# Kernel optimization log

Hardware: AMD Instinct MI355X
Metric: run time of the kernel (lower is better)

The kernel has to match this reference:

```python
import jax, jax.numpy as jnp
import numpy as np

WH, WW = 8, 8
N_TOK = WH * WW
NUM_HEADS = 4
DIM = 128
B_WIN = 4096  # num_windows * B
NW = 64       # windows per image (for mask)


def _make_rel_tables():
    # relative coords table (1, 2*Wh-1, 2*Ww-1, 2), log-spaced as in SwinV2
    ch = np.arange(-(WH - 1), WH, dtype=np.float32)
    cw = np.arange(-(WW - 1), WW, dtype=np.float32)
    t = np.stack(np.meshgrid(ch, cw, indexing='ij'), axis=-1)[None]  # (1,15,15,2)
    t[..., 0] /= (WH - 1)
    t[..., 1] /= (WW - 1)
    t *= 8
    t = np.sign(t) * np.log2(np.abs(t) + 1.0) / np.log2(8)
    # relative position index (N, N)
    coords = np.stack(np.meshgrid(np.arange(WH), np.arange(WW), indexing='ij'))
    cf = coords.reshape(2, -1)
    rel = cf[:, :, None] - cf[:, None, :]
    rel = rel.transpose(1, 2, 0).copy()
    rel[:, :, 0] += WH - 1
    rel[:, :, 1] += WW - 1
    rel[:, :, 0] *= 2 * WW - 1
    idx = rel.sum(-1).astype(np.int32)
    return jnp.asarray(t), jnp.asarray(idx)


def setup_inputs() -> dict:
    key = jax.random.key(0)
    ks = jax.random.split(key, 8)
    table, idx = _make_rel_tables()
    return {
        'x': jax.random.normal(ks[0], (B_WIN, N_TOK, DIM), jnp.float32),
        'context': jax.random.normal(ks[1], (B_WIN, N_TOK, DIM), jnp.float32),
        'mask': jnp.zeros((NW, N_TOK, N_TOK), jnp.float32),
        'q_w': jax.random.normal(ks[2], (DIM, DIM), jnp.float32) * 0.02,
        'q_b': jnp.zeros((DIM,), jnp.float32),
        'kv_w': jax.random.normal(ks[3], (2 * DIM, DIM), jnp.float32) * 0.02,
        'v_b': jnp.zeros((DIM,), jnp.float32),
        'logit_scale': jnp.full((NUM_HEADS, 1, 1), np.log(10.0), jnp.float32),
        'cpb_w1': jax.random.normal(ks[4], (512, 2), jnp.float32) * 0.02,
        'cpb_b1': jnp.zeros((512,), jnp.float32),
        'cpb_w2': jax.random.normal(ks[5], (NUM_HEADS, 512), jnp.float32) * 0.02,
        'proj_w': jax.random.normal(ks[6], (DIM, DIM), jnp.float32) * 0.02,
        'proj_b': jnp.zeros((DIM,), jnp.float32),
        'rel_coords_table': table,
        'rel_pos_index': idx,
    }


def _l2norm(t, eps=1e-12):
    return t / jnp.maximum(jnp.linalg.norm(t, axis=-1, keepdims=True), eps)


def reference(x, context, mask, q_w, q_b, kv_w, v_b, logit_scale,
              cpb_w1, cpb_b1, cpb_w2, proj_w, proj_b,
              rel_coords_table, rel_pos_index):
    B_, N, C = x.shape
    H = NUM_HEADS
    hd = C // H
    # projections (kv bias = [zeros_like(v_b); v_b])
    q = x @ q_w.T + q_b
    kv_bias = jnp.concatenate([jnp.zeros_like(v_b), v_b])
    kv = context @ kv_w.T + kv_bias
    q = q.reshape(B_, N, H, hd).transpose(0, 2, 1, 3)          # (B_,H,N,hd)
    kv = kv.reshape(B_, N, 2, H, hd).transpose(2, 0, 3, 1, 4)  # (2,B_,H,N,hd)
    k, v = kv[0], kv[1]
    # cosine attention with clamped learned scale
    attn = jnp.einsum('bhnd,bhmd->bhnm', _l2norm(q), _l2norm(k))
    scale = jnp.exp(jnp.minimum(logit_scale, np.log(1.0 / 0.01)))  # (H,1,1)
    attn = attn * scale[None]
    # CPB-MLP relative position bias
    hidd = jax.nn.relu(rel_coords_table @ cpb_w1.T + cpb_b1)   # (1,15,15,512)
    table = (hidd @ cpb_w2.T).reshape(-1, H)                   # ((2Wh-1)(2Ww-1), H)
    bias = table[rel_pos_index.reshape(-1)].reshape(N, N, H)
    bias = 16.0 * jax.nn.sigmoid(bias.transpose(2, 0, 1))      # (H,N,N)
    attn = attn + bias[None]
    # shift mask
    nW = mask.shape[0]
    attn = attn.reshape(B_ // nW, nW, H, N, N) + mask[None, :, None]
    attn = attn.reshape(B_, H, N, N)
    attn = jax.nn.softmax(attn, axis=-1)
    out = jnp.einsum('bhnm,bhmd->bhnd', attn, v)
    out = out.transpose(0, 2, 1, 3).reshape(B_, N, C)
    return out @ proj_w.T + proj_b
```

## Files before the change

kernel.cpp:

```cpp
#include <hip/hip_runtime.h>
#include <hip/hip_bf16.h>

#define NT 64
#define DIM 128

typedef __attribute__((ext_vector_type(8))) short short8;
typedef __attribute__((ext_vector_type(4))) short short4v;
typedef __attribute__((ext_vector_type(8))) __bf16 bf16x8;
typedef __attribute__((ext_vector_type(4))) float floatx4;

#define MFMA(a,b,c) __builtin_amdgcn_mfma_f32_16x16x32_bf16(a,b,c,0,0,0)
#define SWZ(idx, row) ((idx) ^ (((row)&7)<<3))

__device__ __forceinline__ short bfbits(float f) {
  return __builtin_bit_cast(short, (__bf16)f);
}

__device__ __forceinline__ bf16x8 frag_bf(const short* __restrict__ p) {
  return __builtin_bit_cast(bf16x8, *(const short8*)p);
}

__device__ __forceinline__ short8 pack8(float4 a, float4 b) {
  short8 v;
  v[0]=bfbits(a.x); v[1]=bfbits(a.y); v[2]=bfbits(a.z); v[3]=bfbits(a.w);
  v[4]=bfbits(b.x); v[5]=bfbits(b.y); v[6]=bfbits(b.z); v[7]=bfbits(b.w);
  return v;
}

__global__ void prep_kernel(const float* __restrict__ table,
                            const float* __restrict__ w1,
                            const float* __restrict__ b1,
                            const float* __restrict__ w2,
                            const int*   __restrict__ idx,
                            const float* __restrict__ q_w,
                            const float* __restrict__ kv_w,
                            const float* __restrict__ proj_w,
                            float* __restrict__ bias_packed,
                            short* __restrict__ wbf) {
  int t = threadIdx.x;
  if (blockIdx.x == 0) {
    __shared__ float logits[225][4];
    if (t < 225) {
      float t0 = table[2*t], t1 = table[2*t+1];
      float a0=0.f, a1=0.f, a2=0.f, a3=0.f;
      for (int j = 0; j < 512; ++j) {
        float h = fmaxf(0.f, t0 * w1[2*j] + t1 * w1[2*j+1] + b1[j]);
        a0 += h * w2[j];
        a1 += h * w2[512 + j];
        a2 += h * w2[1024 + j];
        a3 += h * w2[1536 + j];
      }
      logits[t][0]=a0; logits[t][1]=a1; logits[t][2]=a2; logits[t][3]=a3;
    }
    __syncthreads();
    for (int f = t; f < 16384; f += 256) {
      int i    = f & 3;
      int lane = (f >> 2) & 63;
      int nt   = (f >> 8) & 3;
      int mt   = (f >> 10) & 3;
      int h    = (f >> 12) & 3;
      int r = mt*16 + (lane >> 4)*4 + i;
      int c = nt*16 + (lane & 15);
      int p = idx[r*64 + c];
      float v = logits[p][h];
      bias_packed[f] = 16.f / (1.f + __expf(-v));
    }
  } else {
    int gidx = (blockIdx.x - 1) * 4096 + t * 16;
    const float* src; int off;
    if (gidx < 16384)      { src = q_w;    off = gidx; }
    else if (gidx < 49152) { src = kv_w;   off = gidx - 16384; }
    else                   { src = proj_w; off = gidx - 49152; }
    const float4* s = (const float4*)(src + off);
    short* dst = wbf + gidx;
#pragma unroll
    for (int i = 0; i < 2; ++i)
      *(short8*)(dst + i*8) = pack8(s[2*i], s[2*i+1]);
  }
}

__global__ __launch_bounds__(512, 4)
void swin_ctx_attn_kernel(const float* __restrict__ x, const float* __restrict__ ctx,
                          const float* __restrict__ mask,
                          const short* __restrict__ wq, const float* __restrict__ q_b,
                          const short* __restrict__ wkv, const float* __restrict__ v_b,
                          const float* __restrict__ logit_scale,
                          const short* __restrict__ wproj, const float* __restrict__ proj_b,
                          const float* __restrict__ bias_p,
                          float* __restrict__ out) {
  __shared__ short lds[40960] __attribute__((aligned(16)));
  const int tid  = threadIdx.x;
  const int lane = tid & 63;
  const int wv   = tid >> 6;
  const int h    = wv >> 1;
  const int s    = wv & 1;
  const int b    = blockIdx.x;
  const int lr   = lane & 15;
  const int lg   = lane >> 4;

  short* sx     = lds;
  short* scx    = lds + 8192;
  short* qn     = lds + 16384 + h*6144;
  short* kn     = qn + 2048;
  short* vT     = qn + 4096;
  short* attnb  = qn;
  short* outp_l = sx;

  const float* xw = x   + (size_t)b*(NT*DIM);
  const float* cw = ctx + (size_t)b*(NT*DIM);

  {
    const int sr = tid >> 3, sc0 = (tid & 7) * 16;
    const float4* xs = (const float4*)(xw + sr*DIM + sc0);
    const float4* cs = (const float4*)(cw + sr*DIM + sc0);
    float4 xr[4], cr[4];
#pragma unroll
    for (int i = 0; i < 4; ++i) xr[i] = xs[i];
#pragma unroll
    for (int i = 0; i < 4; ++i) cr[i] = cs[i];
#pragma unroll
    for (int i = 0; i < 2; ++i)
      *(short8*)(sx + SWZ(sr*128 + sc0 + i*8, sr)) = pack8(xr[2*i], xr[2*i+1]);
#pragma unroll
    for (int i = 0; i < 2; ++i)
      *(short8*)(scx + SWZ(sr*128 + sc0 + i*8, sr)) = pack8(cr[2*i], cr[2*i+1]);
  }
  bf16x8 Bq[4][2];
#pragma unroll
  for (int ks = 0; ks < 4; ++ks)
#pragma unroll
    for (int n = 0; n < 2; ++n)
      Bq[ks][n] = frag_bf(wq + (h*32 + n*16 + lr)*DIM + ks*32 + lg*8);
  __syncthreads();

  {
    floatx4 acc[2][2] = {};
    for (int ks = 0; ks < 4; ++ks) {
      bf16x8 A[2];
#pragma unroll
      for (int m = 0; m < 2; ++m) {
        int q = s*32 + m*16 + lr;
        A[m] = frag_bf(sx + SWZ(q*128 + ks*32 + lg*8, q));
      }
#pragma unroll
      for (int n = 0; n < 2; ++n)
#pragma unroll
        for (int m = 0; m < 2; ++m)
          acc[m][n] = MFMA(A[m], Bq[ks][n], acc[m][n]);
    }
    float qb0 = q_b[h*32 + lr], qb1 = q_b[h*32 + 16 + lr];
#pragma unroll
    for (int m = 0; m < 2; ++m) {
      floatx4 ss;
#pragma unroll
      for (int i = 0; i < 4; ++i) {
        acc[m][0][i] += qb0; acc[m][1][i] += qb1;
        ss[i] = acc[m][0][i]*acc[m][0][i] + acc[m][1][i]*acc[m][1][i];
      }
      for (int mm = 1; mm < 16; mm <<= 1)
#pragma unroll
        for (int i = 0; i < 4; ++i) ss[i] += __shfl_xor(ss[i], mm, 64);
#pragma unroll
      for (int i = 0; i < 4; ++i) {
        float sc = 1.0f / fmaxf(sqrtf(ss[i]), 1e-12f);
        int row = s*32 + m*16 + lg*4 + i;
        qn[SWZ(row*32 + lr,      row)] = bfbits(acc[m][0][i] * sc);
        qn[SWZ(row*32 + 16 + lr, row)] = bfbits(acc[m][1][i] * sc);
      }
    }
  }

  {
    floatx4 kacc[2][2] = {}, vacc[2][2] = {};
    for (int ks = 0; ks < 4; ++ks) {
      bf16x8 A[2], Bk[2], Bv[2];
#pragma unroll
      for (int m = 0; m < 2; ++m) {
        int q = s*32 + m*16 + lr;
        A[m] = frag_bf(scx + SWZ(q*128 + ks*32 + lg*8, q));
      }
#pragma unroll
      for (int n = 0; n < 2; ++n) {
        Bk[n] = frag_bf(wkv + (h*32 + n*16 + lr)*DIM + ks*32 + lg*8);
        Bv[n] = frag_bf(wkv + (DIM + h*32 + n*16 + lr)*DIM + ks*32 + lg*8);
      }
#pragma unroll
      for (int n = 0; n < 2; ++n)
#pragma unroll
        for (int m = 0; m < 2; ++m) {
          kacc[m][n] = MFMA(A[m], Bk[n], kacc[m][n]);
          vacc[m][n] = MFMA(A[m], Bv[n], vacc[m][n]);
        }
    }
#pragma unroll
    for (int m = 0; m < 2; ++m) {
      floatx4 ss;
#pragma unroll
      for (int i = 0; i < 4; ++i)
        ss[i] = kacc[m][0][i]*kacc[m][0][i] + kacc[m][1][i]*kacc[m][1][i];
      for (int mm = 1; mm < 16; mm <<= 1)
#pragma unroll
        for (int i = 0; i < 4; ++i) ss[i] += __shfl_xor(ss[i], mm, 64);
#pragma unroll
      for (int i = 0; i < 4; ++i) {
        float sc = 1.0f / fmaxf(sqrtf(ss[i]), 1e-12f);
        int row = s*32 + m*16 + lg*4 + i;
        kn[SWZ(row*32 + lr,      row)] = bfbits(kacc[m][0][i] * sc);
        kn[SWZ(row*32 + 16 + lr, row)] = bfbits(kacc[m][1][i] * sc);
      }
    }
    float vb0 = v_b[h*32 + lr], vb1 = v_b[h*32 + 16 + lr];
#pragma unroll
    for (int m = 0; m < 2; ++m)
#pragma unroll
      for (int n = 0; n < 2; ++n) {
        float vb = n ? vb1 : vb0;
        short4v s4;
#pragma unroll
        for (int i = 0; i < 4; ++i) s4[i] = bfbits(vacc[m][n][i] + vb);
        int d = n*16 + lr, tok0 = s*32 + m*16 + lg*4;
        *(short4v*)(vT + SWZ(d*64 + tok0, d)) = s4;
      }
  }
  __syncthreads();

  floatx4 sacc[2][4] = {};
  {
    bf16x8 A[2], Bf[4];
#pragma unroll
    for (int m = 0; m < 2; ++m) {
      int q = s*32 + m*16 + lr;
      A[m] = frag_bf(qn + SWZ(q*32 + lg*8, q));
    }
#pragma unroll
    for (int n = 0; n < 4; ++n) {
      int r = n*16 + lr;
      Bf[n] = frag_bf(kn + SWZ(r*32 + lg*8, r));
    }
#pragma unroll
    for (int n = 0; n < 4; ++n)
#pragma unroll
      for (int m = 0; m < 2; ++m)
        sacc[m][n] = MFMA(A[m], Bf[n], sacc[m][n]);
  }

  {
    float scl = __expf(fminf(logit_scale[h], 4.605170185988091f));
    int wimg = b & 63;
#pragma unroll
    for (int m = 0; m < 2; ++m)
#pragma unroll
      for (int nt = 0; nt < 4; ++nt) {
        floatx4 bias4 = ((const floatx4*)bias_p)[(h*16 + (s*2+m)*4 + nt)*64 + lane];
#pragma unroll
        for (int i = 0; i < 4; ++i) {
          int r = s*32 + m*16 + lg*4 + i, c = nt*16 + lr;
          sacc[m][nt][i] = sacc[m][nt][i]*scl + bias4[i] + mask[((size_t)wimg*64 + r)*64 + c];
        }
      }
#pragma unroll
    for (int m = 0; m < 2; ++m) {
      floatx4 rmax;
#pragma unroll
      for (int i = 0; i < 4; ++i)
        rmax[i] = fmaxf(fmaxf(sacc[m][0][i], sacc[m][1][i]), fmaxf(sacc[m][2][i], sacc[m][3][i]));
      for (int mm = 1; mm < 16; mm <<= 1)
#pragma unroll
        for (int i = 0; i < 4; ++i) rmax[i] = fmaxf(rmax[i], __shfl_xor(rmax[i], mm, 64));
      floatx4 rsum = {};
#pragma unroll
      for (int nt = 0; nt < 4; ++nt)
#pragma unroll
        for (int i = 0; i < 4; ++i) {
          sacc[m][nt][i] = __expf(sacc[m][nt][i] - rmax[i]);
          rsum[i] += sacc[m][nt][i];
        }
      for (int mm = 1; mm < 16; mm <<= 1)
#pragma unroll
        for (int i = 0; i < 4; ++i) rsum[i] += __shfl_xor(rsum[i], mm, 64);
#pragma unroll
      for (int i = 0; i < 4; ++i) rsum[i] = 1.0f / rsum[i];
#pragma unroll
      for (int nt = 0; nt < 4; ++nt)
#pragma unroll
        for (int i = 0; i < 4; ++i) sacc[m][nt][i] *= rsum[i];
    }
  }
  __syncthreads();

#pragma unroll
  for (int m = 0; m < 2; ++m)
#pragma unroll
    for (int nt = 0; nt < 4; ++nt)
#pragma unroll
      for (int i = 0; i < 4; ++i) {
        int q = s*32 + m*16 + lg*4 + i;
        attnb[SWZ(q*64 + nt*16 + lr, q)] = bfbits(sacc[m][nt][i]);
      }
  asm volatile("s_waitcnt lgkmcnt(0)" ::: "memory");
  __builtin_amdgcn_sched_barrier(0);

  floatx4 oacc[2][2] = {};
#pragma unroll
  for (int ks = 0; ks < 2; ++ks) {
    bf16x8 A[2], Bf[2];
#pragma unroll
    for (int m = 0; m < 2; ++m) {
      int q = s*32 + m*16 + lr;
      A[m] = frag_bf(attnb + SWZ(q*64 + ks*32 + lg*8, q));
    }
#pragma unroll
    for (int n = 0; n < 2; ++n) {
      int d = n*16 + lr;
      Bf[n] = frag_bf(vT + SWZ(d*64 + ks*32 + lg*8, d));
    }
#pragma unroll
    for (int n = 0; n < 2; ++n)
#pragma unroll
      for (int m = 0; m < 2; ++m)
        oacc[m][n] = MFMA(A[m], Bf[n], oacc[m][n]);
  }

#pragma unroll
  for (int m = 0; m < 2; ++m)
#pragma unroll
    for (int n = 0; n < 2; ++n)
#pragma unroll
      for (int i = 0; i < 4; ++i) {
        int q = s*32 + m*16 + lg*4 + i;
        outp_l[SWZ(q*128 + h*32 + n*16 + lr, q)] = bfbits(oacc[m][n][i]);
      }
  __syncthreads();

  {
    floatx4 acc[2][2] = {};
    for (int ks = 0; ks < 4; ++ks) {
      bf16x8 A[2], B[2];
#pragma unroll
      for (int m = 0; m < 2; ++m) {
        int q = s*32 + m*16 + lr;
        A[m] = frag_bf(outp_l + SWZ(q*128 + ks*32 + lg*8, q));
      }
#pragma unroll
      for (int n = 0; n < 2; ++n)
        B[n] = frag_bf(wproj + (h*32 + n*16 + lr)*DIM + ks*32 + lg*8);
#pragma unroll
      for (int n = 0; n < 2; ++n)
#pragma unroll
        for (int m = 0; m < 2; ++m)
          acc[m][n] = MFMA(A[m], B[n], acc[m][n]);
    }
    float pb0 = proj_b[h*32 + lr], pb1 = proj_b[h*32 + 16 + lr];
    float* outp = out + (size_t)b * (NT*DIM);
#pragma unroll
    for (int m = 0; m < 2; ++m)
#pragma unroll
      for (int n = 0; n < 2; ++n) {
        float pb = n ? pb1 : pb0;
#pragma unroll
        for (int i = 0; i < 4; ++i)
          outp[(s*32 + m*16 + lg*4 + i)*DIM + h*32 + n*16 + lr] = acc[m][n][i] + pb;
      }
  }
}

extern "C" void kernel_launch(void* const* d_in, const int* in_sizes, int n_in,
                              void* d_out, int out_size, void* d_ws, size_t ws_size,
                              hipStream_t stream) {
  const float* x     = (const float*)d_in[0];
  const float* ctx   = (const float*)d_in[1];
  const float* mask  = (const float*)d_in[2];
  const float* q_w   = (const float*)d_in[3];
  const float* q_b   = (const float*)d_in[4];
  const float* kv_w  = (const float*)d_in[5];
  const float* v_b   = (const float*)d_in[6];
  const float* ls    = (const float*)d_in[7];
  const float* w1    = (const float*)d_in[8];
  const float* b1    = (const float*)d_in[9];
  const float* w2    = (const float*)d_in[10];
  const float* pw    = (const float*)d_in[11];
  const float* pb    = (const float*)d_in[12];
  const float* table = (const float*)d_in[13];
  const int*   idx   = (const int*)d_in[14];

  float* bias_p = (float*)d_ws;
  short* wbf    = (short*)((char*)d_ws + 65536);
  short* wq     = wbf;
  short* wkv    = wbf + 16384;
  short* wproj  = wbf + 49152;
  int B = in_sizes[0] / (NT * DIM);

  prep_kernel<<<17, 256, 0, stream>>>(table, w1, b1, w2, idx, q_w, kv_w, pw,
                                      bias_p, wbf);
  swin_ctx_attn_kernel<<<B, 512, 0, stream>>>(x, ctx, mask, wq, q_b, wkv, v_b,
                                              ls, wproj, pb, bias_p, (float*)d_out);
}
```

Before: 267.3 us.

## Compute attention transposed with register-resident Q and P to shrink LDS

The kernel now computes Q and scores in transposed form (W·X^T, K·Q^T), so normalized Q and the softmax probabilities stay in registers and are repacked into MFMA operands with cross-lane shuffles and byte permutes instead of round-tripping through LDS. The logit scale is folded into the Q normalization, the row-sum reciprocal is applied after the PV product, and bias/mask loads become vectorized to match the new layout. LDS shrinks from 80KB to 48KB by reusing the x/context buffers for V^T and the attention output, and launch bounds rise to 6 blocks per SM. The cost is extra shuffles and register pressure under the tighter occupancy target, plus an additional barrier.

```diff
diff --git a/kernel.cpp b/kernel.cpp
--- a/kernel.cpp
+++ b/kernel.cpp
@@ -8,6 +8,7 @@
 typedef __attribute__((ext_vector_type(4))) short short4v;
 typedef __attribute__((ext_vector_type(8))) __bf16 bf16x8;
 typedef __attribute__((ext_vector_type(4))) float floatx4;
+typedef __attribute__((ext_vector_type(4))) unsigned uintx4;
 
 #define MFMA(a,b,c) __builtin_amdgcn_mfma_f32_16x16x32_bf16(a,b,c,0,0,0)
 #define SWZ(idx, row) ((idx) ^ (((row)&7)<<3))
@@ -15,11 +16,13 @@
 __device__ __forceinline__ short bfbits(float f) {
   return __builtin_bit_cast(short, (__bf16)f);
 }
-
+__device__ __forceinline__ unsigned pk2(float lo, float hi) {
+  return (unsigned)(unsigned short)__builtin_bit_cast(unsigned short, (__bf16)lo)
+       | ((unsigned)(unsigned short)__builtin_bit_cast(unsigned short, (__bf16)hi) << 16);
+}
 __device__ __forceinline__ bf16x8 frag_bf(const short* __restrict__ p) {
   return __builtin_bit_cast(bf16x8, *(const short8*)p);
 }
-
 __device__ __forceinline__ short8 pack8(float4 a, float4 b) {
   short8 v;
   v[0]=bfbits(a.x); v[1]=bfbits(a.y); v[2]=bfbits(a.z); v[3]=bfbits(a.w);
@@ -56,12 +59,12 @@
     for (int f = t; f < 16384; f += 256) {
       int i    = f & 3;
       int lane = (f >> 2) & 63;
-      int nt   = (f >> 8) & 3;
-      int mt   = (f >> 10) & 3;
-      int h    = (f >> 12) & 3;
-      int r = mt*16 + (lane >> 4)*4 + i;
-      int c = nt*16 + (lane & 15);
-      int p = idx[r*64 + c];
+      int qt   = (f >> 8) & 3;
+      int mk   = (f >> 10) & 3;
+      int h    = f >> 12;
+      int q = qt*16 + (lane & 15);
+      int k = mk*16 + ((lane >> 4) & 3)*4 + i;
+      int p = idx[q*64 + k];
       float v = logits[p][h];
       bias_packed[f] = 16.f / (1.f + __expf(-v));
     }
@@ -79,7 +82,7 @@
   }
 }
 
-__global__ __launch_bounds__(512, 4)
+__global__ __launch_bounds__(512, 6)
 void swin_ctx_attn_kernel(const float* __restrict__ x, const float* __restrict__ ctx,
                           const float* __restrict__ mask,
                           const short* __restrict__ wq, const float* __restrict__ q_b,
@@ -88,7 +91,7 @@
                           const short* __restrict__ wproj, const float* __restrict__ proj_b,
                           const float* __restrict__ bias_p,
                           float* __restrict__ out) {
-  __shared__ short lds[40960] __attribute__((aligned(16)));
+  __shared__ short lds[24576] __attribute__((aligned(16)));
   const int tid  = threadIdx.x;
   const int lane = tid & 63;
   const int wv   = tid >> 6;
@@ -98,13 +101,12 @@
   const int lr   = lane & 15;
   const int lg   = lane >> 4;
 
-  short* sx     = lds;
-  short* scx    = lds + 8192;
-  short* qn     = lds + 16384 + h*6144;
-  short* kn     = qn + 2048;
-  short* vT     = qn + 4096;
-  short* attnb  = qn;
-  short* outp_l = sx;
+  short* xb   = lds;
+  short* cb   = lds + 8192;
+  short* kn   = lds + 16384;
+  short* vT   = xb;
+  short* outp = cb;
+  short* knh  = kn + h*2048;
 
   const float* xw = x   + (size_t)b*(NT*DIM);
   const float* cw = ctx + (size_t)b*(NT*DIM);
@@ -120,238 +122,244 @@
     for (int i = 0; i < 4; ++i) cr[i] = cs[i];
 #pragma unroll
     for (int i = 0; i < 2; ++i)
-      *(short8*)(sx + SWZ(sr*128 + sc0 + i*8, sr)) = pack8(xr[2*i], xr[2*i+1]);
+      *(short8*)(xb + SWZ(sr*128 + sc0 + i*8, sr)) = pack8(xr[2*i], xr[2*i+1]);
 #pragma unroll
     for (int i = 0; i < 2; ++i)
-      *(short8*)(scx + SWZ(sr*128 + sc0 + i*8, sr)) = pack8(cr[2*i], cr[2*i+1]);
-  }
-  bf16x8 Bq[4][2];
-#pragma unroll
-  for (int ks = 0; ks < 4; ++ks)
-#pragma unroll
-    for (int n = 0; n < 2; ++n)
-      Bq[ks][n] = frag_bf(wq + (h*32 + n*16 + lr)*DIM + ks*32 + lg*8);
+      *(short8*)(cb + SWZ(sr*128 + sc0 + i*8, sr)) = pack8(cr[2*i], cr[2*i+1]);
+  }
   __syncthreads();
 
-  {
-    floatx4 acc[2][2] = {};
+  const int sA = ((lane & 16) << 1) | (lane & 15);
+  const int sB = sA + 16;
+  const unsigned selp = (lane & 32) ? 0x07060302u : 0x05040100u;
+
+  bf16x8 qB[2];
+  float scl = __expf(fminf(logit_scale[h], 4.605170185988091f));
+  {
+    floatx4 aq[2][2] = {};
     for (int ks = 0; ks < 4; ++ks) {
-      bf16x8 A[2];
+      bf16x8 xf[2], wf[2];
+#pragma unroll
+      for (int n = 0; n < 2; ++n) {
+        int tok = (2*s + n)*16 + lr;
+        xf[n] = frag_bf(xb + SWZ(tok*128 + ks*32 + lg*8, tok));
+      }
+#pragma unroll
+      for (int mc = 0; mc < 2; ++mc)
+        wf[mc] = frag_bf(wq + (h*32 + mc*16 + lr)*DIM + ks*32 + lg*8);
+#pragma unroll
+      for (int mc = 0; mc < 2; ++mc)
+#pragma unroll
+        for (int n = 0; n < 2; ++n)
+          aq[mc][n] = MFMA(wf[mc], xf[n], aq[mc][n]);
+    }
+    floatx4 qb4[2];
+#pragma unroll
+    for (int mc = 0; mc < 2; ++mc)
+      qb4[mc] = *(const floatx4*)(q_b + h*32 + mc*16 + lg*4);
+#pragma unroll
+    for (int n = 0; n < 2; ++n) {
+      float ss = 0.f;
+#pragma unroll
+      for (int mc = 0; mc < 2; ++mc)
+#pragma unroll
+        for (int i = 0; i < 4; ++i) {
+          aq[mc][n][i] += qb4[mc][i];
+          ss += aq[mc][n][i]*aq[mc][n][i];
+        }
+      ss += __shfl_xor(ss, 16, 64);
+      ss += __shfl_xor(ss, 32, 64);
+      float sc = scl / fmaxf(sqrtf(ss), 1e-12f);
+#pragma unroll
+      for (int mc = 0; mc < 2; ++mc)
+#pragma unroll
+        for (int i = 0; i < 4; ++i) aq[mc][n][i] *= sc;
+      unsigned pq[4], w[8];
+#pragma unroll
+      for (int i = 0; i < 4; ++i) pq[i] = pk2(aq[0][n][i], aq[1][n][i]);
+#pragma unroll
+      for (int j = 0; j < 8; ++j) w[j] = __shfl(pq[j & 3], (j < 4) ? sA : sB, 64);
+      uintx4 u;
+#pragma unroll
+      for (int t = 0; t < 4; ++t) u[t] = __builtin_amdgcn_perm(w[2*t+1], w[2*t], selp);
+      qB[n] = __builtin_bit_cast(bf16x8, u);
+    }
+  }
+
+  floatx4 ak[2][2] = {}, av[2][2] = {};
+  for (int ks = 0; ks < 4; ++ks) {
+    bf16x8 cf[2], wkf[2], wvf[2];
+#pragma unroll
+    for (int r = 0; r < 2; ++r) {
+      int tok = (2*s + r)*16 + lr;
+      cf[r] = frag_bf(cb + SWZ(tok*128 + ks*32 + lg*8, tok));
+    }
+#pragma unroll
+    for (int mc = 0; mc < 2; ++mc) {
+      wkf[mc] = frag_bf(wkv + (h*32 + mc*16 + lr)*DIM + ks*32 + lg*8);
+      wvf[mc] = frag_bf(wkv + (DIM + h*32 + mc*16 + lr)*DIM + ks*32 + lg*8);
+    }
+#pragma unroll
+    for (int mc = 0; mc < 2; ++mc)
+#pragma unroll
+      for (int n = 0; n < 2; ++n) {
+        ak[mc][n] = MFMA(wkf[mc], cf[n], ak[mc][n]);
+        av[mc][n] = MFMA(cf[mc], wvf[n], av[mc][n]);
+      }
+  }
+#pragma unroll
+  for (int n = 0; n < 2; ++n) {
+    float ss = 0.f;
+#pragma unroll
+    for (int mc = 0; mc < 2; ++mc)
+#pragma unroll
+      for (int i = 0; i < 4; ++i) ss += ak[mc][n][i]*ak[mc][n][i];
+    ss += __shfl_xor(ss, 16, 64);
+    ss += __shfl_xor(ss, 32, 64);
+    float sc = 1.0f / fmaxf(sqrtf(ss), 1e-12f);
+#pragma unroll
+    for (int mc = 0; mc < 2; ++mc)
+#pragma unroll
+      for (int i = 0; i < 4; ++i) ak[mc][n][i] *= sc;
+  }
+#pragma unroll
+  for (int mc = 0; mc < 2; ++mc)
+#pragma unroll
+    for (int n = 0; n < 2; ++n) {
+      int tok = (2*s + n)*16 + lr;
+      short4v t4;
+#pragma unroll
+      for (int i = 0; i < 4; ++i) t4[i] = bfbits(ak[mc][n][i]);
+      *(short4v*)(knh + SWZ(tok*32 + mc*16 + lg*4, tok)) = t4;
+    }
+  __syncthreads();
+
+  {
+    float vb0 = v_b[h*32 + lr], vb1 = v_b[h*32 + 16 + lr];
+#pragma unroll
+    for (int m = 0; m < 2; ++m)
+#pragma unroll
+      for (int n = 0; n < 2; ++n) {
+        int chG = h*32 + n*16 + lr;
+        float vb = n ? vb1 : vb0;
+        short4v t4;
+#pragma unroll
+        for (int i = 0; i < 4; ++i) t4[i] = bfbits(av[m][n][i] + vb);
+        *(short4v*)(vT + SWZ(chG*64 + s*32 + m*16 + lg*4, chG)) = t4;
+      }
+  }
+  __syncthreads();
+
+  floatx4 st[4][2] = {};
+  {
+    bf16x8 kf[4];
+#pragma unroll
+    for (int mk = 0; mk < 4; ++mk) {
+      int tok = mk*16 + lr;
+      kf[mk] = frag_bf(knh + SWZ(tok*32 + lg*8, tok));
+    }
+#pragma unroll
+    for (int mk = 0; mk < 4; ++mk)
+#pragma unroll
+      for (int n = 0; n < 2; ++n)
+        st[mk][n] = MFMA(kf[mk], qB[n], st[mk][n]);
+  }
+
+  float rinv[2];
+  {
+    int wimg = b & 63;
+#pragma unroll
+    for (int n = 0; n < 2; ++n) {
+      int qcol = (2*s + n)*16 + lr;
+#pragma unroll
+      for (int mk = 0; mk < 4; ++mk) {
+        floatx4 b4 = ((const floatx4*)bias_p)[((h*4 + mk)*4 + (2*s + n))*64 + lane];
+        floatx4 m4 = *(const floatx4*)(mask + ((size_t)wimg*64 + qcol)*64 + mk*16 + lg*4);
+#pragma unroll
+        for (int i = 0; i < 4; ++i) st[mk][n][i] += b4[i] + m4[i];
+      }
+      float mx = st[0][n][0];
+#pragma unroll
+      for (int mk = 0; mk < 4; ++mk)
+#pragma unroll
+        for (int i = 0; i < 4; ++i) mx = fmaxf(mx, st[mk][n][i]);
+      mx = fmaxf(mx, __shfl_xor(mx, 16, 64));
+      mx = fmaxf(mx, __shfl_xor(mx, 32, 64));
+      float sum = 0.f;
+#pragma unroll
+      for (int mk = 0; mk < 4; ++mk)
+#pragma unroll
+        for (int i = 0; i < 4; ++i) {
+          st[mk][n][i] = __expf(st[mk][n][i] - mx);
+          sum += st[mk][n][i];
+        }
+      sum += __shfl_xor(sum, 16, 64);
+      sum += __shfl_xor(sum, 32, 64);
+      rinv[n] = 1.0f / sum;
+    }
+  }
+
+  floatx4 ot[2][2] = {};
+#pragma unroll
+  for (int kk = 0; kk < 2; ++kk) {
+    bf16x8 pB[2];
+#pragma unroll
+    for (int n = 0; n < 2; ++n) {
+      unsigned pp[4], w[8];
+#pragma unroll
+      for (int i = 0; i < 4; ++i) pp[i] = pk2(st[2*kk][n][i], st[2*kk+1][n][i]);
+#pragma unroll
+      for (int j = 0; j < 8; ++j) w[j] = __shfl(pp[j & 3], (j < 4) ? sA : sB, 64);
+      uintx4 u;
+#pragma unroll
+      for (int t = 0; t < 4; ++t) u[t] = __builtin_amdgcn_perm(w[2*t+1], w[2*t], selp);
+      pB[n] = __builtin_bit_cast(bf16x8, u);
+    }
+    bf16x8 vf[2];
+#pragma unroll
+    for (int mo = 0; mo < 2; ++mo) {
+      int chG = h*32 + mo*16 + lr;
+      vf[mo] = frag_bf(vT + SWZ(chG*64 + kk*32 + lg*8, chG));
+    }
+#pragma unroll
+    for (int mo = 0; mo < 2; ++mo)
+#pragma unroll
+      for (int n = 0; n < 2; ++n)
+        ot[mo][n] = MFMA(vf[mo], pB[n], ot[mo][n]);
+  }
+
+#pragma unroll
+  for (int mo = 0; mo < 2; ++mo)
+#pragma unroll
+    for (int n = 0; n < 2; ++n) {
+      int tok = (2*s + n)*16 + lr;
+      short4v t4;
+#pragma unroll
+      for (int i = 0; i < 4; ++i) t4[i] = bfbits(ot[mo][n][i] * rinv[n]);
+      *(short4v*)(outp + SWZ(tok*128 + h*32 + mo*16 + lg*4, tok)) = t4;
+    }
+  __syncthreads();
+
+  {
+    floatx4 ap[2][2] = {};
+    for (int ks = 0; ks < 4; ++ks) {
+      bf16x8 of[2], wpf[2];
 #pragma unroll
       for (int m = 0; m < 2; ++m) {
-        int q = s*32 + m*16 + lr;
-        A[m] = frag_bf(sx + SWZ(q*128 + ks*32 + lg*8, q));
+        int tok = s*32 + m*16 + lr;
+        of[m] = frag_bf(outp + SWZ(tok*128 + ks*32 + lg*8, tok));
       }
 #pragma unroll
       for (int n = 0; n < 2; ++n)
-#pragma unroll
-        for (int m = 0; m < 2; ++m)
-          acc[m][n] = MFMA(A[m], Bq[ks][n], acc[m][n]);
-    }
-    float qb0 = q_b[h*32 + lr], qb1 = q_b[h*32 + 16 + lr];
-#pragma unroll
-    for (int m = 0; m < 2; ++m) {
-      floatx4 ss;
-#pragma unroll
-      for (int i = 0; i < 4; ++i) {
-        acc[m][0][i] += qb0; acc[m][1][i] += qb1;
-        ss[i] = acc[m][0][i]*acc[m][0][i] + acc[m][1][i]*acc[m][1][i];
-      }
-      for (int mm = 1; mm < 16; mm <<= 1)
-#pragma unroll
-        for (int i = 0; i < 4; ++i) ss[i] += __shfl_xor(ss[i], mm, 64);
-#pragma unroll
-      for (int i = 0; i < 4; ++i) {
-        float sc = 1.0f / fmaxf(sqrtf(ss[i]), 1e-12f);
-        int row = s*32 + m*16 + lg*4 + i;
-        qn[SWZ(row*32 + lr,      row)] = bfbits(acc[m][0][i] * sc);
-        qn[SWZ(row*32 + 16 + lr, row)] = bfbits(acc[m][1][i] * sc);
-      }
-    }
-  }
-
-  {
-    floatx4 kacc[2][2] = {}, vacc[2][2] = {};
-    for (int ks = 0; ks < 4; ++ks) {
-      bf16x8 A[2], Bk[2], Bv[2];
-#pragma unroll
-      for (int m = 0; m < 2; ++m) {
-        int q = s*32 + m*16 + lr;
-        A[m] = frag_bf(scx + SWZ(q*128 + ks*32 + lg*8, q));
-      }
-#pragma unroll
-      for (int n = 0; n < 2; ++n) {
-        Bk[n] = frag_bf(wkv + (h*32 + n*16 + lr)*DIM + ks*32 + lg*8);
-        Bv[n] = frag_bf(wkv + (DIM + h*32 + n*16 + lr)*DIM + ks*32 + lg*8);
-      }
-#pragma unroll
-      for (int n = 0; n < 2; ++n)
-#pragma unroll
-        for (int m = 0; m < 2; ++m) {
-          kacc[m][n] = MFMA(A[m], Bk[n], kacc[m][n]);
-          vacc[m][n] = MFMA(A[m], Bv[n], vacc[m][n]);
-        }
-    }
-#pragma unroll
-    for (int m = 0; m < 2; ++m) {
-      floatx4 ss;
-#pragma unroll
-      for (int i = 0; i < 4; ++i)
-        ss[i] = kacc[m][0][i]*kacc[m][0][i] + kacc[m][1][i]*kacc[m][1][i];
-      for (int mm = 1; mm < 16; mm <<= 1)
-#pragma unroll
-        for (int i = 0; i < 4; ++i) ss[i] += __shfl_xor(ss[i], mm, 64);
-#pragma unroll
-      for (int i = 0; i < 4; ++i) {
-        float sc = 1.0f / fmaxf(sqrtf(ss[i]), 1e-12f);
-        int row = s*32 + m*16 + lg*4 + i;
-        kn[SWZ(row*32 + lr,      row)] = bfbits(kacc[m][0][i] * sc);
-        kn[SWZ(row*32 + 16 + lr, row)] = bfbits(kacc[m][1][i] * sc);
-      }
-    }
-    float vb0 = v_b[h*32 + lr], vb1 = v_b[h*32 + 16 + lr];
-#pragma unroll
-    for (int m = 0; m < 2; ++m)
-#pragma unroll
-      for (int n = 0; n < 2; ++n) {
-        float vb = n ? vb1 : vb0;
-        short4v s4;
-#pragma unroll
-        for (int i = 0; i < 4; ++i) s4[i] = bfbits(vacc[m][n][i] + vb);
-        int d = n*16 + lr, tok0 = s*32 + m*16 + lg*4;
-        *(short4v*)(vT + SWZ(d*64 + tok0, d)) = s4;
-      }
-  }
-  __syncthreads();
-
-  floatx4 sacc[2][4] = {};
-  {
-    bf16x8 A[2], Bf[4];
-#pragma unroll
-    for (int m = 0; m < 2; ++m) {
-      int q = s*32 + m*16 + lr;
-      A[m] = frag_bf(qn + SWZ(q*32 + lg*8, q));
-    }
-#pragma unroll
-    for (int n = 0; n < 4; ++n) {
-      int r = n*16 + lr;
-      Bf[n] = frag_bf(kn + SWZ(r*32 + lg*8, r));
-    }
-#pragma unroll
-    for (int n = 0; n < 4; ++n)
+        wpf[n] = frag_bf(wproj + (h*32 + n*16 + lr)*DIM + ks*32 + lg*8);
 #pragma unroll
       for (int m = 0; m < 2; ++m)
-        sacc[m][n] = MFMA(A[m], Bf[n], sacc[m][n]);
-  }
-
-  {
-    float scl = __expf(fminf(logit_scale[h], 4.605170185988091f));
-    int wimg = b & 63;
-#pragma unroll
-    for (int m = 0; m < 2; ++m)
-#pragma unroll
-      for (int nt = 0; nt < 4; ++nt) {
-        floatx4 bias4 = ((const floatx4*)bias_p)[(h*16 + (s*2+m)*4 + nt)*64 + lane];
-#pragma unroll
-        for (int i = 0; i < 4; ++i) {
-          int r = s*32 + m*16 + lg*4 + i, c = nt*16 + lr;
-          sacc[m][nt][i] = sacc[m][nt][i]*scl + bias4[i] + mask[((size_t)wimg*64 + r)*64 + c];
-        }
-      }
-#pragma unroll
-    for (int m = 0; m < 2; ++m) {
-      floatx4 rmax;
-#pragma unroll
-      for (int i = 0; i < 4; ++i)
-        rmax[i] = fmaxf(fmaxf(sacc[m][0][i], sacc[m][1][i]), fmaxf(sacc[m][2][i], sacc[m][3][i]));
-      for (int mm = 1; mm < 16; mm <<= 1)
-#pragma unroll
-        for (int i = 0; i < 4; ++i) rmax[i] = fmaxf(rmax[i], __shfl_xor(rmax[i], mm, 64));
-      floatx4 rsum = {};
-#pragma unroll
-      for (int nt = 0; nt < 4; ++nt)
-#pragma unroll
-        for (int i = 0; i < 4; ++i) {
-          sacc[m][nt][i] = __expf(sacc[m][nt][i] - rmax[i]);
-          rsum[i] += sacc[m][nt][i];
-        }
-      for (int mm = 1; mm < 16; mm <<= 1)
-#pragma unroll
-        for (int i = 0; i < 4; ++i) rsum[i] += __shfl_xor(rsum[i], mm, 64);
-#pragma unroll
-      for (int i = 0; i < 4; ++i) rsum[i] = 1.0f / rsum[i];
-#pragma unroll
-      for (int nt = 0; nt < 4; ++nt)
-#pragma unroll
-        for (int i = 0; i < 4; ++i) sacc[m][nt][i] *= rsum[i];
-    }
-  }
-  __syncthreads();
-
-#pragma unroll
-  for (int m = 0; m < 2; ++m)
-#pragma unroll
-    for (int nt = 0; nt < 4; ++nt)
-#pragma unroll
-      for (int i = 0; i < 4; ++i) {
-        int q = s*32 + m*16 + lg*4 + i;
-        attnb[SWZ(q*64 + nt*16 + lr, q)] = bfbits(sacc[m][nt][i]);
-      }
-  asm volatile("s_waitcnt lgkmcnt(0)" ::: "memory");
-  __builtin_amdgcn_sched_barrier(0);
-
-  floatx4 oacc[2][2] = {};
-#pragma unroll
-  for (int ks = 0; ks < 2; ++ks) {
-    bf16x8 A[2], Bf[2];
-#pragma unroll
-    for (int m = 0; m < 2; ++m) {
-      int q = s*32 + m*16 + lr;
-      A[m] = frag_bf(attnb + SWZ(q*64 + ks*32 + lg*8, q));
-    }
-#pragma unroll
-    for (int n = 0; n < 2; ++n) {
-      int d = n*16 + lr;
-      Bf[n] = frag_bf(vT + SWZ(d*64 + ks*32 + lg*8, d));
-    }
-#pragma unroll
-    for (int n = 0; n < 2; ++n)
-#pragma unroll
-      for (int m = 0; m < 2; ++m)
-        oacc[m][n] = MFMA(A[m], Bf[n], oacc[m][n]);
-  }
-
-#pragma unroll
-  for (int m = 0; m < 2; ++m)
-#pragma unroll
-    for (int n = 0; n < 2; ++n)
-#pragma unroll
-      for (int i = 0; i < 4; ++i) {
-        int q = s*32 + m*16 + lg*4 + i;
-        outp_l[SWZ(q*128 + h*32 + n*16 + lr, q)] = bfbits(oacc[m][n][i]);
-      }
-  __syncthreads();
-
-  {
-    floatx4 acc[2][2] = {};
-    for (int ks = 0; ks < 4; ++ks) {
-      bf16x8 A[2], B[2];
-#pragma unroll
-      for (int m = 0; m < 2; ++m) {
-        int q = s*32 + m*16 + lr;
-        A[m] = frag_bf(outp_l + SWZ(q*128 + ks*32 + lg*8, q));
-      }
-#pragma unroll
-      for (int n = 0; n < 2; ++n)
-        B[n] = frag_bf(wproj + (h*32 + n*16 + lr)*DIM + ks*32 + lg*8);
-#pragma unroll
-      for (int n = 0; n < 2; ++n)
-#pragma unroll
-        for (int m = 0; m < 2; ++m)
-          acc[m][n] = MFMA(A[m], B[n], acc[m][n]);
+#pragma unroll
+        for (int n = 0; n < 2; ++n)
+          ap[m][n] = MFMA(of[m], wpf[n], ap[m][n]);
     }
     float pb0 = proj_b[h*32 + lr], pb1 = proj_b[h*32 + 16 + lr];
-    float* outp = out + (size_t)b * (NT*DIM);
+    float* op = out + (size_t)b * (NT*DIM);
 #pragma unroll
     for (int m = 0; m < 2; ++m)
 #pragma unroll
@@ -359,7 +367,7 @@
         float pb = n ? pb1 : pb0;
 #pragma unroll
         for (int i = 0; i < 4; ++i)
-          outp[(s*32 + m*16 + lg*4 + i)*DIM + h*32 + n*16 + lr] = acc[m][n][i] + pb;
+          op[(s*32 + m*16 + lg*4 + i)*DIM + h*32 + n*16 + lr] = ap[m][n][i] + pb;
       }
   }
 }
```

New measurement: 343.8 us. 1.29x slower.

## Use one wave per head over all 64 tokens with 256-thread blocks

Applied to the files above, without the earlier changes.

Restructures the attention kernel from eight waves (head × token half) to four waves, each handling one head across all 64 tokens, and shrinks LDS from 80KB to 48KB by reusing the x/context buffers for normalized Q/K, probabilities and head outputs. The logit scale is folded into the Q normalization, the V projection is computed first, and MFMA blocks are wrapped in s_setprio. Each wave now reuses its weight fragments across four M tiles and the kernel needs fewer barriers, at the cost of higher register pressure and fewer waves per block to hide latency.

```diff
diff --git a/kernel.cpp b/kernel.cpp
--- a/kernel.cpp
+++ b/kernel.cpp
@@ -15,11 +15,9 @@
 __device__ __forceinline__ short bfbits(float f) {
   return __builtin_bit_cast(short, (__bf16)f);
 }
-
 __device__ __forceinline__ bf16x8 frag_bf(const short* __restrict__ p) {
   return __builtin_bit_cast(bf16x8, *(const short8*)p);
 }
-
 __device__ __forceinline__ short8 pack8(float4 a, float4 b) {
   short8 v;
   v[0]=bfbits(a.x); v[1]=bfbits(a.y); v[2]=bfbits(a.z); v[3]=bfbits(a.w);
@@ -58,7 +56,7 @@
       int lane = (f >> 2) & 63;
       int nt   = (f >> 8) & 3;
       int mt   = (f >> 10) & 3;
-      int h    = (f >> 12) & 3;
+      int h    = f >> 12;
       int r = mt*16 + (lane >> 4)*4 + i;
       int c = nt*16 + (lane & 15);
       int p = idx[r*64 + c];
@@ -79,7 +77,7 @@
   }
 }
 
-__global__ __launch_bounds__(512, 4)
+__global__ __launch_bounds__(256, 3)
 void swin_ctx_attn_kernel(const float* __restrict__ x, const float* __restrict__ ctx,
                           const float* __restrict__ mask,
                           const short* __restrict__ wq, const float* __restrict__ q_b,
@@ -88,182 +86,205 @@
                           const short* __restrict__ wproj, const float* __restrict__ proj_b,
                           const float* __restrict__ bias_p,
                           float* __restrict__ out) {
-  __shared__ short lds[40960] __attribute__((aligned(16)));
+  __shared__ short lds[24576] __attribute__((aligned(16)));
   const int tid  = threadIdx.x;
   const int lane = tid & 63;
-  const int wv   = tid >> 6;
-  const int h    = wv >> 1;
-  const int s    = wv & 1;
+  const int h    = tid >> 6;
   const int b    = blockIdx.x;
   const int lr   = lane & 15;
   const int lg   = lane >> 4;
 
-  short* sx     = lds;
-  short* scx    = lds + 8192;
-  short* qn     = lds + 16384 + h*6144;
-  short* kn     = qn + 2048;
-  short* vT     = qn + 4096;
-  short* attnb  = qn;
-  short* outp_l = sx;
-
-  const float* xw = x   + (size_t)b*(NT*DIM);
-  const float* cw = ctx + (size_t)b*(NT*DIM);
-
-  {
-    const int sr = tid >> 3, sc0 = (tid & 7) * 16;
-    const float4* xs = (const float4*)(xw + sr*DIM + sc0);
-    const float4* cs = (const float4*)(cw + sr*DIM + sc0);
-    float4 xr[4], cr[4];
-#pragma unroll
-    for (int i = 0; i < 4; ++i) xr[i] = xs[i];
-#pragma unroll
-    for (int i = 0; i < 4; ++i) cr[i] = cs[i];
-#pragma unroll
-    for (int i = 0; i < 2; ++i)
-      *(short8*)(sx + SWZ(sr*128 + sc0 + i*8, sr)) = pack8(xr[2*i], xr[2*i+1]);
-#pragma unroll
-    for (int i = 0; i < 2; ++i)
-      *(short8*)(scx + SWZ(sr*128 + sc0 + i*8, sr)) = pack8(cr[2*i], cr[2*i+1]);
-  }
-  bf16x8 Bq[4][2];
-#pragma unroll
-  for (int ks = 0; ks < 4; ++ks)
-#pragma unroll
-    for (int n = 0; n < 2; ++n)
-      Bq[ks][n] = frag_bf(wq + (h*32 + n*16 + lr)*DIM + ks*32 + lg*8);
+  short* xb   = lds;
+  short* cbuf = lds + 8192;
+  short* vbuf = lds + 16384;
+  short* qnh  = xb   + h*2048;
+  short* knh  = cbuf + h*2048;
+  short* vth  = vbuf + h*2048;
+
+  {
+    const int sr = tid >> 2, c0 = (tid & 3) * 32;
+    const float4* xs = (const float4*)(x   + (size_t)b*(NT*DIM) + sr*DIM + c0);
+    const float4* cs = (const float4*)(ctx + (size_t)b*(NT*DIM) + sr*DIM + c0);
+    float4 xr[8], cr[8];
+#pragma unroll
+    for (int i = 0; i < 8; ++i) xr[i] = xs[i];
+#pragma unroll
+    for (int i = 0; i < 8; ++i) cr[i] = cs[i];
+#pragma unroll
+    for (int j = 0; j < 4; ++j)
+      *(short8*)(xb + SWZ(sr*128 + c0 + j*8, sr)) = pack8(xr[2*j], xr[2*j+1]);
+#pragma unroll
+    for (int j = 0; j < 4; ++j)
+      *(short8*)(cbuf + SWZ(sr*128 + c0 + j*8, sr)) = pack8(cr[2*j], cr[2*j+1]);
+  }
   __syncthreads();
 
-  {
-    floatx4 acc[2][2] = {};
+  const float scl = __expf(fminf(logit_scale[h], 4.605170185988091f));
+
+  {
+    floatx4 av[4][2] = {};
     for (int ks = 0; ks < 4; ++ks) {
-      bf16x8 A[2];
-#pragma unroll
-      for (int m = 0; m < 2; ++m) {
-        int q = s*32 + m*16 + lr;
-        A[m] = frag_bf(sx + SWZ(q*128 + ks*32 + lg*8, q));
-      }
-#pragma unroll
-      for (int n = 0; n < 2; ++n)
-#pragma unroll
-        for (int m = 0; m < 2; ++m)
-          acc[m][n] = MFMA(A[m], Bq[ks][n], acc[m][n]);
-    }
-    float qb0 = q_b[h*32 + lr], qb1 = q_b[h*32 + 16 + lr];
-#pragma unroll
-    for (int m = 0; m < 2; ++m) {
-      floatx4 ss;
-#pragma unroll
-      for (int i = 0; i < 4; ++i) {
-        acc[m][0][i] += qb0; acc[m][1][i] += qb1;
-        ss[i] = acc[m][0][i]*acc[m][0][i] + acc[m][1][i]*acc[m][1][i];
-      }
-      for (int mm = 1; mm < 16; mm <<= 1)
-#pragma unroll
-        for (int i = 0; i < 4; ++i) ss[i] += __shfl_xor(ss[i], mm, 64);
-#pragma unroll
-      for (int i = 0; i < 4; ++i) {
-        float sc = 1.0f / fmaxf(sqrtf(ss[i]), 1e-12f);
-        int row = s*32 + m*16 + lg*4 + i;
-        qn[SWZ(row*32 + lr,      row)] = bfbits(acc[m][0][i] * sc);
-        qn[SWZ(row*32 + 16 + lr, row)] = bfbits(acc[m][1][i] * sc);
-      }
-    }
-  }
-
-  {
-    floatx4 kacc[2][2] = {}, vacc[2][2] = {};
-    for (int ks = 0; ks < 4; ++ks) {
-      bf16x8 A[2], Bk[2], Bv[2];
-#pragma unroll
-      for (int m = 0; m < 2; ++m) {
-        int q = s*32 + m*16 + lr;
-        A[m] = frag_bf(scx + SWZ(q*128 + ks*32 + lg*8, q));
-      }
-#pragma unroll
-      for (int n = 0; n < 2; ++n) {
-        Bk[n] = frag_bf(wkv + (h*32 + n*16 + lr)*DIM + ks*32 + lg*8);
-        Bv[n] = frag_bf(wkv + (DIM + h*32 + n*16 + lr)*DIM + ks*32 + lg*8);
-      }
-#pragma unroll
-      for (int n = 0; n < 2; ++n)
-#pragma unroll
-        for (int m = 0; m < 2; ++m) {
-          kacc[m][n] = MFMA(A[m], Bk[n], kacc[m][n]);
-          vacc[m][n] = MFMA(A[m], Bv[n], vacc[m][n]);
-        }
-    }
-#pragma unroll
-    for (int m = 0; m < 2; ++m) {
-      floatx4 ss;
-#pragma unroll
-      for (int i = 0; i < 4; ++i)
-        ss[i] = kacc[m][0][i]*kacc[m][0][i] + kacc[m][1][i]*kacc[m][1][i];
-      for (int mm = 1; mm < 16; mm <<= 1)
-#pragma unroll
-        for (int i = 0; i < 4; ++i) ss[i] += __shfl_xor(ss[i], mm, 64);
-#pragma unroll
-      for (int i = 0; i < 4; ++i) {
-        float sc = 1.0f / fmaxf(sqrtf(ss[i]), 1e-12f);
-        int row = s*32 + m*16 + lg*4 + i;
-        kn[SWZ(row*32 + lr,      row)] = bfbits(kacc[m][0][i] * sc);
-        kn[SWZ(row*32 + 16 + lr, row)] = bfbits(kacc[m][1][i] * sc);
-      }
+      bf16x8 A[4], W[2];
+#pragma unroll
+      for (int m = 0; m < 4; ++m) {
+        int tok = m*16 + lr;
+        A[m] = frag_bf(cbuf + SWZ(tok*128 + ks*32 + lg*8, tok));
+      }
+#pragma unroll
+      for (int n = 0; n < 2; ++n)
+        W[n] = frag_bf(wkv + (DIM + h*32 + n*16 + lr)*DIM + ks*32 + lg*8);
+      __builtin_amdgcn_s_setprio(1);
+#pragma unroll
+      for (int n = 0; n < 2; ++n)
+#pragma unroll
+        for (int m = 0; m < 4; ++m)
+          av[m][n] = MFMA(A[m], W[n], av[m][n]);
+      __builtin_amdgcn_s_setprio(0);
     }
     float vb0 = v_b[h*32 + lr], vb1 = v_b[h*32 + 16 + lr];
 #pragma unroll
-    for (int m = 0; m < 2; ++m)
+    for (int m = 0; m < 4; ++m)
 #pragma unroll
       for (int n = 0; n < 2; ++n) {
         float vb = n ? vb1 : vb0;
-        short4v s4;
-#pragma unroll
-        for (int i = 0; i < 4; ++i) s4[i] = bfbits(vacc[m][n][i] + vb);
-        int d = n*16 + lr, tok0 = s*32 + m*16 + lg*4;
-        *(short4v*)(vT + SWZ(d*64 + tok0, d)) = s4;
-      }
+        short4v t4;
+#pragma unroll
+        for (int i = 0; i < 4; ++i) t4[i] = bfbits(av[m][n][i] + vb);
+        int ch = n*16 + lr;
+        *(short4v*)(vth + SWZ(ch*64 + m*16 + lg*4, ch)) = t4;
+      }
+  }
+
+  floatx4 qc[4][2] = {};
+  {
+    for (int ks = 0; ks < 4; ++ks) {
+      bf16x8 A[4], W[2];
+#pragma unroll
+      for (int m = 0; m < 4; ++m) {
+        int tok = m*16 + lr;
+        A[m] = frag_bf(xb + SWZ(tok*128 + ks*32 + lg*8, tok));
+      }
+#pragma unroll
+      for (int n = 0; n < 2; ++n)
+        W[n] = frag_bf(wq + (h*32 + n*16 + lr)*DIM + ks*32 + lg*8);
+      __builtin_amdgcn_s_setprio(1);
+#pragma unroll
+      for (int n = 0; n < 2; ++n)
+#pragma unroll
+        for (int m = 0; m < 4; ++m)
+          qc[m][n] = MFMA(A[m], W[n], qc[m][n]);
+      __builtin_amdgcn_s_setprio(0);
+    }
+    float qb0 = q_b[h*32 + lr], qb1 = q_b[h*32 + 16 + lr];
+#pragma unroll
+    for (int m = 0; m < 4; ++m) {
+      floatx4 ss;
+#pragma unroll
+      for (int i = 0; i < 4; ++i) {
+        qc[m][0][i] += qb0; qc[m][1][i] += qb1;
+        ss[i] = qc[m][0][i]*qc[m][0][i] + qc[m][1][i]*qc[m][1][i];
+      }
+      for (int mm = 1; mm < 16; mm <<= 1)
+#pragma unroll
+        for (int i = 0; i < 4; ++i) ss[i] += __shfl_xor(ss[i], mm, 64);
+#pragma unroll
+      for (int i = 0; i < 4; ++i) {
+        float sc = scl / fmaxf(sqrtf(ss[i]), 1e-12f);
+        qc[m][0][i] *= sc; qc[m][1][i] *= sc;
+      }
+    }
+  }
+
+  floatx4 kc[4][2] = {};
+  {
+    for (int ks = 0; ks < 4; ++ks) {
+      bf16x8 A[4], W[2];
+#pragma unroll
+      for (int m = 0; m < 4; ++m) {
+        int tok = m*16 + lr;
+        A[m] = frag_bf(cbuf + SWZ(tok*128 + ks*32 + lg*8, tok));
+      }
+#pragma unroll
+      for (int n = 0; n < 2; ++n)
+        W[n] = frag_bf(wkv + (h*32 + n*16 + lr)*DIM + ks*32 + lg*8);
+      __builtin_amdgcn_s_setprio(1);
+#pragma unroll
+      for (int n = 0; n < 2; ++n)
+#pragma unroll
+        for (int m = 0; m < 4; ++m)
+          kc[m][n] = MFMA(A[m], W[n], kc[m][n]);
+      __builtin_amdgcn_s_setprio(0);
+    }
+#pragma unroll
+    for (int m = 0; m < 4; ++m) {
+      floatx4 ss;
+#pragma unroll
+      for (int i = 0; i < 4; ++i)
+        ss[i] = kc[m][0][i]*kc[m][0][i] + kc[m][1][i]*kc[m][1][i];
+      for (int mm = 1; mm < 16; mm <<= 1)
+#pragma unroll
+        for (int i = 0; i < 4; ++i) ss[i] += __shfl_xor(ss[i], mm, 64);
+#pragma unroll
+      for (int i = 0; i < 4; ++i) {
+        float sc = 1.0f / fmaxf(sqrtf(ss[i]), 1e-12f);
+        kc[m][0][i] *= sc; kc[m][1][i] *= sc;
+      }
+    }
   }
   __syncthreads();
 
-  floatx4 sacc[2][4] = {};
-  {
-    bf16x8 A[2], Bf[4];
-#pragma unroll
-    for (int m = 0; m < 2; ++m) {
-      int q = s*32 + m*16 + lr;
-      A[m] = frag_bf(qn + SWZ(q*32 + lg*8, q));
-    }
-#pragma unroll
-    for (int n = 0; n < 4; ++n) {
-      int r = n*16 + lr;
-      Bf[n] = frag_bf(kn + SWZ(r*32 + lg*8, r));
-    }
-#pragma unroll
-    for (int n = 0; n < 4; ++n)
-#pragma unroll
-      for (int m = 0; m < 2; ++m)
-        sacc[m][n] = MFMA(A[m], Bf[n], sacc[m][n]);
-  }
-
-  {
-    float scl = __expf(fminf(logit_scale[h], 4.605170185988091f));
+#pragma unroll
+  for (int m = 0; m < 4; ++m)
+#pragma unroll
+    for (int n = 0; n < 2; ++n)
+#pragma unroll
+      for (int i = 0; i < 4; ++i) {
+        int tok = m*16 + lg*4 + i;
+        qnh[SWZ(tok*32 + n*16 + lr, tok)] = bfbits(qc[m][n][i]);
+        knh[SWZ(tok*32 + n*16 + lr, tok)] = bfbits(kc[m][n][i]);
+      }
+  asm volatile("s_waitcnt lgkmcnt(0)" ::: "memory");
+  __builtin_amdgcn_sched_barrier(0);
+
+  floatx4 sacc[4][4] = {};
+  {
+    bf16x8 qA[4];
+#pragma unroll
+    for (int m = 0; m < 4; ++m) {
+      int tok = m*16 + lr;
+      qA[m] = frag_bf(qnh + SWZ(tok*32 + lg*8, tok));
+    }
+    __builtin_amdgcn_s_setprio(1);
+#pragma unroll
+    for (int nt = 0; nt < 4; ++nt) {
+      int ktok = nt*16 + lr;
+      bf16x8 kB = frag_bf(knh + SWZ(ktok*32 + lg*8, ktok));
+#pragma unroll
+      for (int m = 0; m < 4; ++m)
+        sacc[m][nt] = MFMA(qA[m], kB, sacc[m][nt]);
+    }
+    __builtin_amdgcn_s_setprio(0);
+  }
+
+  {
     int wimg = b & 63;
 #pragma unroll
-    for (int m = 0; m < 2; ++m)
+    for (int mt = 0; mt < 4; ++mt)
 #pragma unroll
       for (int nt = 0; nt < 4; ++nt) {
-        floatx4 bias4 = ((const floatx4*)bias_p)[(h*16 + (s*2+m)*4 + nt)*64 + lane];
+        floatx4 bias4 = ((const floatx4*)bias_p)[(h*16 + mt*4 + nt)*64 + lane];
 #pragma unroll
         for (int i = 0; i < 4; ++i) {
-          int r = s*32 + m*16 + lg*4 + i, c = nt*16 + lr;
-          sacc[m][nt][i] = sacc[m][nt][i]*scl + bias4[i] + mask[((size_t)wimg*64 + r)*64 + c];
+          int r = mt*16 + lg*4 + i, c = nt*16 + lr;
+          sacc[mt][nt][i] += bias4[i] + mask[((size_t)wimg*64 + r)*64 + c];
         }
       }
 #pragma unroll
-    for (int m = 0; m < 2; ++m) {
+    for (int mt = 0; mt < 4; ++mt) {
       floatx4 rmax;
 #pragma unroll
       for (int i = 0; i < 4; ++i)
-        rmax[i] = fmaxf(fmaxf(sacc[m][0][i], sacc[m][1][i]), fmaxf(sacc[m][2][i], sacc[m][3][i]));
+        rmax[i] = fmaxf(fmaxf(sacc[mt][0][i], sacc[mt][1][i]), fmaxf(sacc[mt][2][i], sacc[mt][3][i]));
       for (int mm = 1; mm < 16; mm <<= 1)
 #pragma unroll
         for (int i = 0; i < 4; ++i) rmax[i] = fmaxf(rmax[i], __shfl_xor(rmax[i], mm, 64));
@@ -272,8 +293,8 @@
       for (int nt = 0; nt < 4; ++nt)
 #pragma unroll
         for (int i = 0; i < 4; ++i) {
-          sacc[m][nt][i] = __expf(sacc[m][nt][i] - rmax[i]);
-          rsum[i] += sacc[m][nt][i];
+          sacc[mt][nt][i] = __expf(sacc[mt][nt][i] - rmax[i]);
+          rsum[i] += sacc[mt][nt][i];
         }
       for (int mm = 1; mm < 16; mm <<= 1)
 #pragma unroll
@@ -283,83 +304,90 @@
 #pragma unroll
       for (int nt = 0; nt < 4; ++nt)
 #pragma unroll
-        for (int i = 0; i < 4; ++i) sacc[m][nt][i] *= rsum[i];
-    }
-  }
-  __syncthreads();
-
-#pragma unroll
-  for (int m = 0; m < 2; ++m)
-#pragma unroll
-    for (int nt = 0; nt < 4; ++nt)
-#pragma unroll
-      for (int i = 0; i < 4; ++i) {
-        int q = s*32 + m*16 + lg*4 + i;
-        attnb[SWZ(q*64 + nt*16 + lr, q)] = bfbits(sacc[m][nt][i]);
-      }
+        for (int i = 0; i < 4; ++i) sacc[mt][nt][i] *= rsum[i];
+    }
+  }
+
+#pragma unroll
+  for (int mt = 0; mt < 4; ++mt)
+#pragma unroll
+    for (int nt = 0; nt < 4; ++nt) {
+      short* reg = (nt < 2) ? qnh : knh;
+#pragma unroll
+      for (int i = 0; i < 4; ++i) {
+        int tok = mt*16 + lg*4 + i;
+        reg[SWZ(tok*32 + (nt & 1)*16 + lr, tok)] = bfbits(sacc[mt][nt][i]);
+      }
+    }
   asm volatile("s_waitcnt lgkmcnt(0)" ::: "memory");
   __builtin_amdgcn_sched_barrier(0);
 
-  floatx4 oacc[2][2] = {};
+  floatx4 oacc[4][2] = {};
 #pragma unroll
   for (int ks = 0; ks < 2; ++ks) {
-    bf16x8 A[2], Bf[2];
-#pragma unroll
-    for (int m = 0; m < 2; ++m) {
-      int q = s*32 + m*16 + lr;
-      A[m] = frag_bf(attnb + SWZ(q*64 + ks*32 + lg*8, q));
+    const short* preg = ks ? knh : qnh;
+    bf16x8 pA[4], vB[2];
+#pragma unroll
+    for (int m = 0; m < 4; ++m) {
+      int tok = m*16 + lr;
+      pA[m] = frag_bf(preg + SWZ(tok*32 + lg*8, tok));
     }
 #pragma unroll
     for (int n = 0; n < 2; ++n) {
-      int d = n*16 + lr;
-      Bf[n] = frag_bf(vT + SWZ(d*64 + ks*32 + lg*8, d));
-    }
+      int ch = n*16 + lr;
+      vB[n] = frag_bf(vth + SWZ(ch*64 + ks*32 + lg*8, ch));
+    }
+    __builtin_amdgcn_s_setprio(1);
 #pragma unroll
     for (int n = 0; n < 2; ++n)
 #pragma unroll
-      for (int m = 0; m < 2; ++m)
-        oacc[m][n] = MFMA(A[m], Bf[n], oacc[m][n]);
-  }
-
-#pragma unroll
-  for (int m = 0; m < 2; ++m)
+      for (int m = 0; m < 4; ++m)
+        oacc[m][n] = MFMA(pA[m], vB[n], oacc[m][n]);
+    __builtin_amdgcn_s_setprio(0);
+  }
+
+#pragma unroll
+  for (int m = 0; m < 4; ++m)
 #pragma unroll
     for (int n = 0; n < 2; ++n)
 #pragma unroll
       for (int i = 0; i < 4; ++i) {
-        int q = s*32 + m*16 + lg*4 + i;
-        outp_l[SWZ(q*128 + h*32 + n*16 + lr, q)] = bfbits(oacc[m][n][i]);
+        int tok = m*16 + lg*4 + i;
+        vth[SWZ(tok*32 + n*16 + lr, tok)] = bfbits(oacc[m][n][i]);
       }
   __syncthreads();
 
   {
-    floatx4 acc[2][2] = {};
+    floatx4 pc[4][2] = {};
     for (int ks = 0; ks < 4; ++ks) {
-      bf16x8 A[2], B[2];
-#pragma unroll
-      for (int m = 0; m < 2; ++m) {
-        int q = s*32 + m*16 + lr;
-        A[m] = frag_bf(outp_l + SWZ(q*128 + ks*32 + lg*8, q));
-      }
-#pragma unroll
-      for (int n = 0; n < 2; ++n)
-        B[n] = frag_bf(wproj + (h*32 + n*16 + lr)*DIM + ks*32 + lg*8);
-#pragma unroll
-      for (int n = 0; n < 2; ++n)
-#pragma unroll
-        for (int m = 0; m < 2; ++m)
-          acc[m][n] = MFMA(A[m], B[n], acc[m][n]);
+      const short* oreg = vbuf + ks*2048;
+      bf16x8 A[4], W[2];
+#pragma unroll
+      for (int m = 0; m < 4; ++m) {
+        int tok = m*16 + lr;
+        A[m] = frag_bf(oreg + SWZ(tok*32 + lg*8, tok));
+      }
+#pragma unroll
+      for (int n = 0; n < 2; ++n)
+        W[n] = frag_bf(wproj + (h*32 + n*16 + lr)*DIM + ks*32 + lg*8);
+      __builtin_amdgcn_s_setprio(1);
+#pragma unroll
+      for (int n = 0; n < 2; ++n)
+#pragma unroll
+        for (int m = 0; m < 4; ++m)
+          pc[m][n] = MFMA(A[m], W[n], pc[m][n]);
+      __builtin_amdgcn_s_setprio(0);
     }
     float pb0 = proj_b[h*32 + lr], pb1 = proj_b[h*32 + 16 + lr];
-    float* outp = out + (size_t)b * (NT*DIM);
-#pragma unroll
-    for (int m = 0; m < 2; ++m)
+    float* op = out + (size_t)b * (NT*DIM);
+#pragma unroll
+    for (int m = 0; m < 4; ++m)
 #pragma unroll
       for (int n = 0; n < 2; ++n) {
         float pb = n ? pb1 : pb0;
 #pragma unroll
         for (int i = 0; i < 4; ++i)
-          outp[(s*32 + m*16 + lg*4 + i)*DIM + h*32 + n*16 + lr] = acc[m][n][i] + pb;
+          op[(m*16 + lg*4 + i)*DIM + h*32 + n*16 + lr] = pc[m][n][i] + pb;
       }
   }
 }
@@ -392,6 +420,6 @@
 
   prep_kernel<<<17, 256, 0, stream>>>(table, w1, b1, w2, idx, q_w, kv_w, pw,
                                       bias_p, wbf);
-  swin_ctx_attn_kernel<<<B, 512, 0, stream>>>(x, ctx, mask, wq, q_b, wkv, v_b,
+  swin_ctx_attn_kernel<<<B, 256, 0, stream>>>(x, ctx, mask, wq, q_b, wkv, v_b,
                                               ls, wproj, pb, bias_p, (float*)d_out);
 }
```

After: 300.5 us. 1.12x slower.
